# Performance work log

Measured on AMD Instinct MI355X. Metric: run time of the kernel, lower is better.

## Reference

```python
import jax, jax.numpy as jnp
import numpy as np

MODEL_DIMS = 2048
BATCH, SEQ = 4, 4096
NFREQ = MODEL_DIMS // 2 + 1  # rfft spectrum length


def setup_inputs() -> dict:
    key = jax.random.key(0)
    k1, k2, k3, k4 = jax.random.split(key, 4)
    x = jax.random.normal(k1, (BATCH, SEQ, MODEL_DIMS), dtype=jnp.float32)
    queries = jax.random.normal(k2, (1, 1, NFREQ), dtype=jnp.float32)
    keyvalues = jax.random.normal(k3, (1, 1, NFREQ), dtype=jnp.float32)
    # torch nn.Linear(model_dims, model_dims, bias=False): weight is [out, in]
    w_out = jax.random.normal(k4, (MODEL_DIMS, MODEL_DIMS), dtype=jnp.float32) * (MODEL_DIMS ** -0.5)
    return {"x": x, "queries": queries, "keyvalues": keyvalues, "w_out": w_out}


def reference(x, queries, keyvalues, w_out):
    # hrr.fft = rfft over feature dim -> complex64 [B, S, NFREQ]
    xhat = jnp.fft.rfft(x, axis=-1)
    q = xhat * queries            # real spectral params broadcast-multiply
    kv = xhat * keyvalues
    kv = jnp.cumsum(kv, axis=1)   # causal prefix sum over sequence
    qv = q * kv
    values_hat = jnp.fft.irfft(qv, n=x.shape[-1], axis=-1)  # back to real [B, S, D]
    # torch Linear: y = x @ W^T
    return jnp.einsum('bsd,ed->bse', values_hat, w_out)
```

## Files before the change

### kernel.cpp

```cpp
#include <hip/hip_runtime.h>
#include <hip/hip_bf16.h>
#include <stdint.h>

#define BATCH 4
#define SEQ   4096
#define DIM   2048
#define NFREQ 1025
#define NCPLX 1024
#define ROWS  (BATCH*SEQ)

#define SCH  16
#define NSC  (SEQ/SCH)
#define NSCG 16
#define NGRP (NSC/NSCG)

#define SPEC_STRIDE 257

typedef __bf16 bf16x8 __attribute__((ext_vector_type(8)));
typedef float  f32x4  __attribute__((ext_vector_type(4)));

__device__ __forceinline__ int drev4(int n) {
  return ((n&3)<<8) | (((n>>2)&3)<<6) | (((n>>4)&3)<<4) | (((n>>6)&3)<<2) | ((n>>8)&3);
}
#define ZI(i) ((i) + ((i)>>4))

__device__ __forceinline__ float2 cmulf(float2 a, float2 b) {
  return make_float2(a.x*b.x - a.y*b.y, a.x*b.y + a.y*b.x);
}

__device__ __forceinline__ unsigned short f2bf(float f) {
  union { float f; unsigned u; } v; v.f = f;
  unsigned r = v.u + 0x7fffu + ((v.u >> 16) & 1u);
  return (unsigned short)(r >> 16);
}
__device__ __forceinline__ unsigned packbf(float2 v) {
  return (unsigned)f2bf(v.x) | ((unsigned)f2bf(v.y) << 16);
}
__device__ __forceinline__ float2 unpackbf(unsigned u) {
  union { unsigned u; float f; } a, b;
  a.u = u << 16; b.u = u & 0xffff0000u;
  return make_float2(a.f, b.f);
}

template<int INV>
__device__ __forceinline__ void fft_stages_tw(float2* z, int tid, const float2* tw1) {
  {
    int b4 = tid*4;
    float2 x0=z[ZI(b4)], x1=z[ZI(b4+1)], x2=z[ZI(b4+2)], x3=z[ZI(b4+3)];
    float2 a = make_float2(x0.x+x2.x, x0.y+x2.y), b = make_float2(x0.x-x2.x, x0.y-x2.y);
    float2 c = make_float2(x1.x+x3.x, x1.y+x3.y), d = make_float2(x1.x-x3.x, x1.y-x3.y);
    z[ZI(b4)]   = make_float2(a.x+c.x, a.y+c.y);
    z[ZI(b4+2)] = make_float2(a.x-c.x, a.y-c.y);
    if (!INV) { z[ZI(b4+1)] = make_float2(b.x+d.y, b.y-d.x);
                z[ZI(b4+3)] = make_float2(b.x-d.y, b.y+d.x); }
    else      { z[ZI(b4+1)] = make_float2(b.x-d.y, b.y+d.x);
                z[ZI(b4+3)] = make_float2(b.x+d.y, b.y-d.x); }
  }
  __syncthreads();
#pragma unroll
  for (int s = 0; s < 4; ++s) {
    const int lq = 2 + 2*s;
    const int q  = 1 << lq;
    int j = tid & (q-1), g = tid >> lq;
    int base = (g << (lq+2)) + j;
    float2 w1 = tw1[s]; if (INV) w1.y = -w1.y;
    float2 w2 = cmulf(w1, w1), w3 = cmulf(w2, w1);
    float2 x0 = z[ZI(base)];
    float2 x1 = cmulf(z[ZI(base+q)],   w1);
    float2 x2 = cmulf(z[ZI(base+2*q)], w2);
    float2 x3 = cmulf(z[ZI(base+3*q)], w3);
    float2 a = make_float2(x0.x+x2.x, x0.y+x2.y), b = make_float2(x0.x-x2.x, x0.y-x2.y);
    float2 c = make_float2(x1.x+x3.x, x1.y+x3.y), d = make_float2(x1.x-x3.x, x1.y-x3.y);
    z[ZI(base)]     = make_float2(a.x+c.x, a.y+c.y);
    z[ZI(base+2*q)] = make_float2(a.x-c.x, a.y-c.y);
    if (!INV) { z[ZI(base+q)]   = make_float2(b.x+d.y, b.y-d.x);
                z[ZI(base+3*q)] = make_float2(b.x-d.y, b.y+d.x); }
    else      { z[ZI(base+q)]   = make_float2(b.x-d.y, b.y+d.x);
                z[ZI(base+3*q)] = make_float2(b.x+d.y, b.y-d.x); }
    __syncthreads();
  }
}

__device__ __forceinline__ void make_tw1(int tid, float2* tw1) {
#pragma unroll
  for (int s = 0; s < 4; ++s) {
    const int lq = 2 + 2*s;
    const int q  = 1 << lq;
    int j = tid & (q-1);
    float ang = -6.2831853071795864769f * (float)j / (float)(4*q);
    float sw, cw; __sincosf(ang, &sw, &cw);
    tw1[s] = make_float2(cw, sw);
  }
}

__global__ __launch_bounds__(256) void fwd_fused(const float* __restrict__ x,
                                                 const float* __restrict__ kvs,
                                                 uint4* __restrict__ spec,
                                                 float2* __restrict__ partial) {
  __shared__ float2 z[ZI(1023)+2];
  const int tid = threadIdx.x;
  const int sc = blockIdx.x & (NSC-1), b = blockIdx.x >> 8;

  float2 tw1[4];
  make_tw1(tid, tw1);
  const int kA = tid, kB = tid + 256;
  float swA, cwA, swB, cwB;
  __sincosf(-3.14159265358979323846f * (float)kA / 1024.0f, &swA, &cwA);
  __sincosf(-3.14159265358979323846f * (float)kB / 1024.0f, &swB, &cwB);
  int id0 = ZI(drev4(2*tid)),     id1 = ZI(drev4(2*tid+1));
  int id2 = ZI(drev4(2*tid+512)), id3 = ZI(drev4(2*tid+513));

  float2 sA={0,0}, sAp={0,0}, sB={0,0}, sBp={0,0}, s5={0,0};

  const size_t row0 = (size_t)b*SEQ + (size_t)sc*SCH;
  const float* xrow = x + row0*DIM;
  float4 c0 = ((const float4*)xrow)[tid];
  float4 c1 = ((const float4*)xrow)[tid + 256];

  for (int s = 0; s < SCH; ++s) {
    float4 n0f, n1f;
    if (s+1 < SCH) {
      const float* nx = xrow + (size_t)(s+1)*DIM;
      n0f = ((const float4*)nx)[tid]; n1f = ((const float4*)nx)[tid + 256];
    }
    z[id0] = make_float2(c0.x, c0.y); z[id1] = make_float2(c0.z, c0.w);
    z[id2] = make_float2(c1.x, c1.y); z[id3] = make_float2(c1.z, c1.w);
    __syncthreads();
    fft_stages_tw<0>(z, tid, tw1);
    float2 ZkA = z[ZI(kA)], ZnA = z[ZI((NCPLX - kA) & (NCPLX-1))];
    float2 ZkB = z[ZI(kB)], ZnB = z[ZI(768 - tid)];
    float Er = 0.5f*(ZkA.x + ZnA.x), Ei = 0.5f*(ZkA.y - ZnA.y);
    float dr = 0.5f*(ZkA.x - ZnA.x), di = 0.5f*(ZkA.y + ZnA.y);
    float2 vA  = make_float2( Er + cwA*di + swA*dr,  Ei + swA*di - cwA*dr);
    float2 vAp = make_float2( Er - cwA*di - swA*dr, -Ei + swA*di - cwA*dr);
    float Fr = 0.5f*(ZkB.x + ZnB.x), Fi = 0.5f*(ZkB.y - ZnB.y);
    float er = 0.5f*(ZkB.x - ZnB.x), ei = 0.5f*(ZkB.y + ZnB.y);
    float2 vB  = make_float2( Fr + cwB*ei + swB*er,  Fi + swB*ei - cwB*er);
    float2 vBp = make_float2( Fr - cwB*ei - swB*er, -Fi + swB*ei - cwB*er);
    sA.x += vA.x;  sA.y += vA.y;   sAp.x += vAp.x; sAp.y += vAp.y;
    sB.x += vB.x;  sB.y += vB.y;   sBp.x += vBp.x; sBp.y += vBp.y;
    uint4* sprow = spec + (row0 + s) * SPEC_STRIDE;
    sprow[tid] = make_uint4(packbf(vA), packbf(vAp), packbf(vB), packbf(vBp));
    if (tid == 0) {
      float2 Z5 = z[ZI(512)];
      float2 v5 = make_float2(Z5.x, -Z5.y);
      s5.x += v5.x; s5.y += v5.y;
      ((unsigned*)(sprow + 256))[0] = packbf(v5);
    }
    __syncthreads();
    c0 = n0f; c1 = n1f;
  }
  float2* pp = partial + ((size_t)(b*NSC + sc)) * NFREQ;
  float kvA = kvs[kA], kvAp = kvs[NCPLX - kA], kvB = kvs[kB], kvBp = kvs[768 - tid];
  pp[kA]          = make_float2(kvA*sA.x,  kvA*sA.y);
  pp[NCPLX - kA]  = make_float2(kvAp*sAp.x, kvAp*sAp.y);
  pp[kB]          = make_float2(kvB*sB.x,  kvB*sB.y);
  pp[768 - tid]   = make_float2(kvBp*sBp.x, kvBp*sBp.y);
  if (tid == 0) { float kv5 = kvs[512]; pp[512] = make_float2(kv5*s5.x, kv5*s5.y); }
}

__global__ __launch_bounds__(256) void scanA(float2* __restrict__ partial,
                                             float2* __restrict__ gtot) {
  int kc = blockIdx.x % 5, g = (blockIdx.x / 5) % NGRP, b = blockIdx.x / (5*NGRP);
  int k = kc*256 + threadIdx.x;
  if (k >= NFREQ) return;
  float2* p = partial + ((size_t)(b*NSC + g*NSCG)) * NFREQ + k;
  float2 run = {0.f, 0.f};
#pragma unroll
  for (int i = 0; i < NSCG; ++i) {
    float2 t = p[(size_t)i*NFREQ];
    p[(size_t)i*NFREQ] = run;
    run.x += t.x; run.y += t.y;
  }
  gtot[((size_t)(b*NGRP + g)) * NFREQ + k] = run;
}

__global__ __launch_bounds__(256) void scanB(float2* __restrict__ gtot) {
  int kc = blockIdx.x % 5, b = blockIdx.x / 5;
  int k = kc*256 + threadIdx.x;
  if (k >= NFREQ) return;
  float2* p = gtot + ((size_t)b*NGRP) * NFREQ + k;
  float2 run = {0.f, 0.f};
#pragma unroll
  for (int g = 0; g < NGRP; ++g) {
    float2 t = p[(size_t)g*NFREQ];
    p[(size_t)g*NFREQ] = run;
    run.x += t.x; run.y += t.y;
  }
}

__global__ __launch_bounds__(256) void inv_fused(const uint4* __restrict__ spec,
                                                 const float* __restrict__ kvs,
                                                 const float* __restrict__ qs_,
                                                 const float2* __restrict__ partial,
                                                 const float2* __restrict__ gtot,
                                                 unsigned short* __restrict__ vout) {
  __shared__ float2 z[ZI(1023)+2];
  const int tid = threadIdx.x;
  const int sc = blockIdx.x & (NSC-1), b = blockIdx.x >> 8;

  float2 tw1[4];
  make_tw1(tid, tw1);
  const int kA = tid, kB = tid + 256;
  float swA, cwA, swB, cwB;
  __sincosf(3.14159265358979323846f * (float)kA / 1024.0f, &swA, &cwA);
  __sincosf(3.14159265358979323846f * (float)kB / 1024.0f, &swB, &cwB);
  int ridA  = ZI(drev4(kA));
  int ridAp = ZI(drev4((NCPLX - kA) & (NCPLX-1)));
  int ridB  = ZI(drev4(kB));
  int ridBp = ZI(drev4(768 - tid));

  float ksA = kvs[kA], ksAp = kvs[NCPLX - kA], ksB = kvs[kB], ksBp = kvs[768 - tid];
  float qsA = qs_[kA], qsAp = qs_[NCPLX - kA], qsB = qs_[kB], qsBp = qs_[768 - tid];

  const float2* pp = partial + ((size_t)(b*NSC + sc)) * NFREQ;
  const float2* gp = gtot + ((size_t)(b*NGRP + (sc >> 4))) * NFREQ;
  float2 CA  = make_float2(pp[kA].x + gp[kA].x,                 pp[kA].y + gp[kA].y);
  float2 CAp = make_float2(pp[NCPLX-kA].x + gp[NCPLX-kA].x,     pp[NCPLX-kA].y + gp[NCPLX-kA].y);
  float2 CB  = make_float2(pp[kB].x + gp[kB].x,                 pp[kB].y + gp[kB].y);
  float2 CBp = make_float2(pp[768-tid].x + gp[768-tid].x,       pp[768-tid].y + gp[768-tid].y);
  float ks5 = kvs[512], qs5 = qs_[512];
  float2 C5 = make_float2(pp[512].x + gp[512].x, pp[512].y + gp[512].y);
  const int rid5 = ZI(drev4(512));

  const size_t row0 = (size_t)b*SEQ + (size_t)sc*SCH;
  const uint4* sprow = spec + row0 * SPEC_STRIDE;
  unsigned* vr = (unsigned*)(vout + row0 * DIM);
  uint4 sp = sprow[tid];
  unsigned spN = ((const unsigned*)(sprow + 256))[0];
  const float scl = 1.0f/1024.0f;

  for (int s = 0; s < SCH; ++s) {
    uint4 spn; unsigned spNn;
    if (s+1 < SCH) {
      const uint4* nr = sprow + (size_t)(s+1) * SPEC_STRIDE;
      spn = nr[tid]; spNn = ((const unsigned*)(nr + 256))[0];
    }
    float2 vA = unpackbf(sp.x), vAp = unpackbf(sp.y);
    float2 vB = unpackbf(sp.z), vBp = unpackbf(sp.w);
    CA.x  += vA.x*ksA;   CA.y  += vA.y*ksA;
    CAp.x += vAp.x*ksAp; CAp.y += vAp.y*ksAp;
    CB.x  += vB.x*ksB;   CB.y  += vB.y*ksB;
    CBp.x += vBp.x*ksBp; CBp.y += vBp.y*ksBp;
    float2 qvA  = make_float2(qsA *(vA.x*CA.x  - vA.y*CA.y),  qsA *(vA.x*CA.y  + vA.y*CA.x));
    float2 qvAp = make_float2(qsAp*(vAp.x*CAp.x- vAp.y*CAp.y),qsAp*(vAp.x*CAp.y+ vAp.y*CAp.x));
    float2 qvB  = make_float2(qsB *(vB.x*CB.x  - vB.y*CB.y),  qsB *(vB.x*CB.y  + vB.y*CB.x));
    float2 qvBp = make_float2(qsBp*(vBp.x*CBp.x- vBp.y*CBp.y),qsBp*(vBp.x*CBp.y+ vBp.y*CBp.x));
    float Er = 0.5f*(qvA.x + qvAp.x), Ei = 0.5f*(qvA.y - qvAp.y);
    float dr = 0.5f*(qvA.x - qvAp.x), di = 0.5f*(qvA.y + qvAp.y);
    float Or = dr*cwA - di*swA, Oi = dr*swA + di*cwA;
    float2 valA  = make_float2(scl*(Er - Oi), scl*( Ei + Or));
    float2 valAp = make_float2(scl*(Er + Oi), scl*(-Ei + Or));
    float Fr = 0.5f*(qvB.x + qvBp.x), Fi = 0.5f*(qvB.y - qvBp.y);
    float er = 0.5f*(qvB.x - qvBp.x), ei = 0.5f*(qvB.y + qvBp.y);
    float Pr = er*cwB - ei*swB, Pi = er*swB + ei*cwB;
    float2 valB  = make_float2(scl*(Fr - Pi), scl*( Fi + Pr));
    float2 valBp = make_float2(scl*(Fr + Pi), scl*(-Fi + Pr));
    z[ridA] = valA; z[ridAp] = valAp; z[ridB] = valB; z[ridBp] = valBp;
    if (tid == 0) {
      float2 v5 = unpackbf(spN);
      C5.x += v5.x*ks5; C5.y += v5.y*ks5;
      float2 qv5 = make_float2(qs5*(v5.x*C5.x - v5.y*C5.y), qs5*(v5.x*C5.y + v5.y*C5.x));
      z[rid5] = make_float2(scl*qv5.x, -scl*qv5.y);
    }
    __syncthreads();
    fft_stages_tw<1>(z, tid, tw1);
    unsigned* vr32 = vr + (size_t)s * (DIM/2);
#pragma unroll
    for (int i = 0; i < 4; ++i) {
      int n = tid + 256*i;
      float2 t2 = z[ZI(n)];
      vr32[n] = packbf(t2);
    }
    __syncthreads();
    sp = spn; spN = spNn;
  }
}

__global__ __launch_bounds__(256) void w_to_bf16(const float* __restrict__ w,
                                                 unsigned short* __restrict__ wb) {
  size_t idx = (size_t)blockIdx.x * 256 + threadIdx.x;
  float4 v = ((const float4*)w)[idx];
  uint2 o;
  o.x = (unsigned)f2bf(v.x) | ((unsigned)f2bf(v.y) << 16);
  o.y = (unsigned)f2bf(v.z) | ((unsigned)f2bf(v.w) << 16);
  ((uint2*)wb)[idx] = o;
}

#define NKT (DIM/64)
#define NIT (NKT/2)

#define BARX() do{ __builtin_amdgcn_s_barrier(); __builtin_amdgcn_sched_barrier(0); }while(0)
#define VMW(N) do{ asm volatile("s_waitcnt vmcnt(" #N ")" ::: "memory"); __builtin_amdgcn_sched_barrier(0); }while(0)

#define LOADA(B_, MH) do{ _Pragma("unroll") for (int m_=0;m_<4;++m_) _Pragma("unroll") for (int kk_=0;kk_<2;++kk_){ \
    int rA_ = wm*64 + m_*16 + l15; \
    aF[m_][kk_] = *(const bf16x8*)(smem + ((B_)*2+(MH))*16384 + rA_*128 + ((kk_*64 + lhi*16) ^ ((rA_&7)<<4))); } }while(0)

#define LOADB(DST, B_, NH) do{ _Pragma("unroll") for (int n_=0;n_<2;++n_) _Pragma("unroll") for (int kk_=0;kk_<2;++kk_){ \
    int rB_ = wn*32 + n_*16 + l15; \
    DST[n_][kk_] = *(const bf16x8*)(smem + 65536 + ((B_)*2+(NH))*16384 + rB_*128 + ((kk_*64 + lhi*16) ^ ((rB_&7)<<4))); } }while(0)

#define MM(MH, NH, BF) do{ __builtin_amdgcn_s_setprio(1); \
    _Pragma("unroll") for (int kk_=0;kk_<2;++kk_) _Pragma("unroll") for (int m_=0;m_<4;++m_) _Pragma("unroll") for (int n_=0;n_<2;++n_) \
      acc[MH][NH][m_][n_] = __builtin_amdgcn_mfma_f32_16x16x32_bf16(aF[m_][kk_], BF[n_][kk_], acc[MH][NH][m_][n_], 0, 0, 0); \
    __builtin_amdgcn_s_setprio(0); }while(0)

#define STAGEH(REG, B_, H_, GP, ROW0, KT) do{ _Pragma("unroll") for (int c_=0;c_<2;++c_){ \
    int ci_ = c_*512 + tid; int r_ = ci_>>3, sl_ = ci_&7; \
    const unsigned short* sp_ = (GP) + (size_t)((ROW0) + (H_)*128 + r_)*DIM + (KT) + ((sl_ ^ (r_&7))*8); \
    __builtin_amdgcn_global_load_lds((const __attribute__((address_space(1))) void*)sp_, \
      (__attribute__((address_space(3))) void*)(smem + (REG) + ((B_)*2+(H_))*16384 + ci_*16), 16, 0, 0); } }while(0)

__global__ __launch_bounds__(512, 2) void gemm256(const unsigned short* __restrict__ A,
                                                  const unsigned short* __restrict__ B,
                                                  float* __restrict__ C) {
  __shared__ __align__(16) char smem[131072];
  const int tid = threadIdx.x;
  const int lane = tid & 63;
  const int wid  = tid >> 6;
  const int wm = wid >> 2, wn = wid & 3;
  const int l15 = lane & 15, lhi = lane >> 4;

  const int bn = blockIdx.x & 7, bm = blockIdx.x >> 3;
  const int m0 = bm * 256, n0 = bn * 256;

  f32x4 acc[2][2][4][2] = {};
  bf16x8 aF[4][2], bF0[2][2], bF1[2][2];

  STAGEH(0,     0,0, A, m0, 0);  STAGEH(65536, 0,0, B, n0, 0);
  STAGEH(65536, 0,1, B, n0, 0);  STAGEH(0,     0,1, A, m0, 0);
  STAGEH(0,     1,0, A, m0, 64); STAGEH(65536, 1,0, B, n0, 64);
  STAGEH(65536, 1,1, B, n0, 64); STAGEH(0,     1,1, A, m0, 64);
  VMW(8);
  BARX();

#pragma unroll 1
  for (int j = 0; j < NIT-1; ++j) {
    const int kA = (2*j+2)*64, kB = (2*j+3)*64;
    LOADA(0,0); LOADB(bF0, 0,0);
    BARX(); MM(0,0,bF0); BARX();
    LOADB(bF1, 0,1);
    STAGEH(0, 0,0, A, m0, kA); STAGEH(65536, 0,0, B, n0, kA);
    BARX(); MM(0,1,bF1); BARX();
    LOADA(0,1);
    STAGEH(65536, 0,1, B, n0, kA);
    BARX(); MM(1,0,bF0); BARX();
    STAGEH(0, 0,1, A, m0, kA);
    VMW(8);
    BARX(); MM(1,1,bF1); BARX();
    LOADA(1,0); LOADB(bF0, 1,0);
    BARX(); MM(0,0,bF0); BARX();
    LOADB(bF1, 1,1);
    STAGEH(0, 1,0, A, m0, kB); STAGEH(65536, 1,0, B, n0, kB);
    BARX(); MM(0,1,bF1); BARX();
    LOADA(1,1);
    STAGEH(65536, 1,1, B, n0, kB);
    BARX(); MM(1,0,bF0); BARX();
    STAGEH(0, 1,1, A, m0, kB);
    VMW(8);
    BARX(); MM(1,1,bF1); BARX();
  }
  LOADA(0,0); LOADB(bF0, 0,0);
  BARX(); MM(0,0,bF0); BARX();
  LOADB(bF1, 0,1);
  BARX(); MM(0,1,bF1); BARX();
  LOADA(0,1);
  BARX(); MM(1,0,bF0); BARX();
  VMW(0);
  BARX(); MM(1,1,bF1); BARX();
  LOADA(1,0); LOADB(bF0, 1,0);
  BARX(); MM(0,0,bF0); BARX();
  LOADB(bF1, 1,1);
  BARX(); MM(0,1,bF1); BARX();
  LOADA(1,1);
  BARX(); MM(1,0,bF0); BARX();
  BARX(); MM(1,1,bF1); BARX();

  const int crow = lhi * 4;
#pragma unroll
  for (int mh = 0; mh < 2; ++mh)
#pragma unroll
    for (int nh = 0; nh < 2; ++nh)
#pragma unroll
      for (int m_ = 0; m_ < 4; ++m_)
#pragma unroll
        for (int n_ = 0; n_ < 2; ++n_) {
          float* cp = C + (size_t)(m0 + mh*128 + wm*64 + m_*16 + crow) * DIM
                        + (n0 + nh*128 + wn*32 + n_*16 + l15);
#pragma unroll
          for (int j2 = 0; j2 < 4; ++j2)
            cp[(size_t)j2 * DIM] = acc[mh][nh][m_][n_][j2];
        }
}

extern "C" void kernel_launch(void* const* d_in, const int* in_sizes, int n_in,
                              void* d_out, int out_size, void* d_ws, size_t ws_size,
                              hipStream_t stream) {
  const float* x    = (const float*)d_in[0];
  const float* qry  = (const float*)d_in[1];
  const float* kvs  = (const float*)d_in[2];
  const float* wout = (const float*)d_in[3];
  float* out = (float*)d_out;

  char* ws = (char*)d_ws;
  size_t off = 0;
  uint4* spec = (uint4*)(ws + off);
  off += (size_t)ROWS * SPEC_STRIDE * sizeof(uint4);
  off = (off + 255) & ~(size_t)255;
  unsigned short* vbf = (unsigned short*)(ws + off);
  off += (size_t)ROWS * DIM * sizeof(unsigned short);
  off = (off + 255) & ~(size_t)255;
  unsigned short* wbf = (unsigned short*)(ws + off);
  off += (size_t)DIM * DIM * sizeof(unsigned short);
  off = (off + 255) & ~(size_t)255;
  float2* partial = (float2*)(ws + off);
  off += (size_t)BATCH * NSC * NFREQ * sizeof(float2);
  off = (off + 255) & ~(size_t)255;
  float2* gtot = (float2*)(ws + off);
  off += (size_t)BATCH * NGRP * NFREQ * sizeof(float2);

  hipLaunchKernelGGL(w_to_bf16, dim3((DIM*DIM)/(256*4)), dim3(256), 0, stream, wout, wbf);
  hipLaunchKernelGGL(fwd_fused, dim3(BATCH*NSC),         dim3(256), 0, stream, x, kvs, spec, partial);
  hipLaunchKernelGGL(scanA,     dim3(BATCH*NGRP*5),      dim3(256), 0, stream, partial, gtot);
  hipLaunchKernelGGL(scanB,     dim3(BATCH*5),           dim3(256), 0, stream, gtot);
  hipLaunchKernelGGL(inv_fused, dim3(BATCH*NSC),         dim3(256), 0, stream, spec, kvs, qry, partial, gtot, vbf);
  hipLaunchKernelGGL(gemm256,   dim3((ROWS/256)*(DIM/256)), dim3(512), 0, stream, vbf, wbf, out);
}
```

Measured before the change: 248.6 us.

## Fold the inverse real FFT into the output projection weights

Instead of running an inverse FFT on every activation row, the change applies a forward real FFT to each row of the weight matrix, scaled so the spectrum rows act as the irfft basis. The inverse kernel now only writes the spectral product's real and imaginary parts as bf16 straight into the GEMM input, which removes the per-row FFT stages, twiddle setup and extra shared-memory passes. The cost is a per-call FFT over the 2048 weight rows, plus extra rounding because spectral values go through bf16 before the matmul. The GEMM block-to-tile mapping is also remapped, probably for cache locality.

```diff
diff --git a/kernel.cpp b/kernel.cpp
--- a/kernel.cpp
+++ b/kernel.cpp
@@ -159,6 +159,63 @@
   if (tid == 0) { float kv5 = kvs[512]; pp[512] = make_float2(kv5*s5.x, kv5*s5.y); }
 }
 
+__global__ __launch_bounds__(256) void wfft(const float* __restrict__ w,
+                                            unsigned short* __restrict__ H) {
+  __shared__ float2 z[ZI(1023)+2];
+  __shared__ __align__(16) unsigned short hrow[2048];
+  const int tid = threadIdx.x;
+  const int e = blockIdx.x;
+
+  float2 tw1[4];
+  make_tw1(tid, tw1);
+  const int kB = tid + 256;
+  float swA, cwA, swB, cwB;
+  __sincosf(-3.14159265358979323846f * (float)tid / 1024.0f, &swA, &cwA);
+  __sincosf(-3.14159265358979323846f * (float)kB  / 1024.0f, &swB, &cwB);
+  int id0 = ZI(drev4(2*tid)),     id1 = ZI(drev4(2*tid+1));
+  int id2 = ZI(drev4(2*tid+512)), id3 = ZI(drev4(2*tid+513));
+
+  const float* wr = w + (size_t)e * DIM;
+  float4 c0 = ((const float4*)wr)[tid];
+  float4 c1 = ((const float4*)wr)[tid + 256];
+  z[id0] = make_float2(c0.x, c0.y); z[id1] = make_float2(c0.z, c0.w);
+  z[id2] = make_float2(c1.x, c1.y); z[id3] = make_float2(c1.z, c1.w);
+  __syncthreads();
+  fft_stages_tw<0>(z, tid, tw1);
+
+  float2 ZkA = z[ZI(tid)], ZnA = z[ZI((NCPLX - tid) & (NCPLX-1))];
+  float2 ZkB = z[ZI(kB)],  ZnB = z[ZI(768 - tid)];
+  float Er = 0.5f*(ZkA.x + ZnA.x), Ei = 0.5f*(ZkA.y - ZnA.y);
+  float dr = 0.5f*(ZkA.x - ZnA.x), di = 0.5f*(ZkA.y + ZnA.y);
+  float2 vA  = make_float2( Er + cwA*di + swA*dr,  Ei + swA*di - cwA*dr);
+  float2 vAp = make_float2( Er - cwA*di - swA*dr, -Ei + swA*di - cwA*dr);
+  float Fr = 0.5f*(ZkB.x + ZnB.x), Fi = 0.5f*(ZkB.y - ZnB.y);
+  float er = 0.5f*(ZkB.x - ZnB.x), ei = 0.5f*(ZkB.y + ZnB.y);
+  float2 vB  = make_float2( Fr + cwB*ei + swB*er,  Fi + swB*ei - cwB*er);
+  float2 vBp = make_float2( Fr - cwB*ei - swB*er, -Fi + swB*ei - cwB*er);
+
+  const float invN = 1.0f/2048.0f, twoN = 2.0f/2048.0f;
+  float aA  = (tid == 0) ? invN : twoN;
+  float aAp = (tid == 0) ? invN : twoN;
+  hrow[tid]        = f2bf(aA  * vA.x);
+  hrow[1024 - tid] = f2bf(aAp * vAp.x);
+  hrow[256 + tid]  = f2bf(twoN * vB.x);
+  hrow[768 - tid]  = f2bf(twoN * vBp.x);
+  if (tid) {
+    hrow[1024 + tid] = f2bf(twoN * vA.y);
+    hrow[2048 - tid] = f2bf(twoN * vAp.y);
+  }
+  hrow[1280 + tid] = f2bf(twoN * vB.y);
+  hrow[1792 - tid] = f2bf(twoN * vBp.y);
+  if (tid == 0) {
+    float2 Z5 = z[ZI(512)];
+    hrow[512]  = f2bf(twoN * Z5.x);
+    hrow[1536] = f2bf(twoN * (-Z5.y));
+  }
+  __syncthreads();
+  ((uint4*)(H + (size_t)e * DIM))[tid] = ((const uint4*)hrow)[tid];
+}
+
 __global__ __launch_bounds__(256) void scanA(float2* __restrict__ partial,
                                              float2* __restrict__ gtot) {
   int kc = blockIdx.x % 5, g = (blockIdx.x / 5) % NGRP, b = blockIdx.x / (5*NGRP);
@@ -194,21 +251,11 @@
                                                  const float* __restrict__ qs_,
                                                  const float2* __restrict__ partial,
                                                  const float2* __restrict__ gtot,
-                                                 unsigned short* __restrict__ vout) {
-  __shared__ float2 z[ZI(1023)+2];
+                                                 unsigned short* __restrict__ G) {
+  __shared__ __align__(16) unsigned short grow[2048];
   const int tid = threadIdx.x;
   const int sc = blockIdx.x & (NSC-1), b = blockIdx.x >> 8;
-
-  float2 tw1[4];
-  make_tw1(tid, tw1);
   const int kA = tid, kB = tid + 256;
-  float swA, cwA, swB, cwB;
-  __sincosf(3.14159265358979323846f * (float)kA / 1024.0f, &swA, &cwA);
-  __sincosf(3.14159265358979323846f * (float)kB / 1024.0f, &swB, &cwB);
-  int ridA  = ZI(drev4(kA));
-  int ridAp = ZI(drev4((NCPLX - kA) & (NCPLX-1)));
-  int ridB  = ZI(drev4(kB));
-  int ridBp = ZI(drev4(768 - tid));
 
   float ksA = kvs[kA], ksAp = kvs[NCPLX - kA], ksB = kvs[kB], ksBp = kvs[768 - tid];
   float qsA = qs_[kA], qsAp = qs_[NCPLX - kA], qsB = qs_[kB], qsBp = qs_[768 - tid];
@@ -221,14 +268,11 @@
   float2 CBp = make_float2(pp[768-tid].x + gp[768-tid].x,       pp[768-tid].y + gp[768-tid].y);
   float ks5 = kvs[512], qs5 = qs_[512];
   float2 C5 = make_float2(pp[512].x + gp[512].x, pp[512].y + gp[512].y);
-  const int rid5 = ZI(drev4(512));
 
   const size_t row0 = (size_t)b*SEQ + (size_t)sc*SCH;
   const uint4* sprow = spec + row0 * SPEC_STRIDE;
-  unsigned* vr = (unsigned*)(vout + row0 * DIM);
   uint4 sp = sprow[tid];
   unsigned spN = ((const unsigned*)(sprow + 256))[0];
-  const float scl = 1.0f/1024.0f;
 
   for (int s = 0; s < SCH; ++s) {
     uint4 spn; unsigned spNn;
@@ -246,45 +290,27 @@
     float2 qvAp = make_float2(qsAp*(vAp.x*CAp.x- vAp.y*CAp.y),qsAp*(vAp.x*CAp.y+ vAp.y*CAp.x));
     float2 qvB  = make_float2(qsB *(vB.x*CB.x  - vB.y*CB.y),  qsB *(vB.x*CB.y  + vB.y*CB.x));
     float2 qvBp = make_float2(qsBp*(vBp.x*CBp.x- vBp.y*CBp.y),qsBp*(vBp.x*CBp.y+ vBp.y*CBp.x));
-    float Er = 0.5f*(qvA.x + qvAp.x), Ei = 0.5f*(qvA.y - qvAp.y);
-    float dr = 0.5f*(qvA.x - qvAp.x), di = 0.5f*(qvA.y + qvAp.y);
-    float Or = dr*cwA - di*swA, Oi = dr*swA + di*cwA;
-    float2 valA  = make_float2(scl*(Er - Oi), scl*( Ei + Or));
-    float2 valAp = make_float2(scl*(Er + Oi), scl*(-Ei + Or));
-    float Fr = 0.5f*(qvB.x + qvBp.x), Fi = 0.5f*(qvB.y - qvBp.y);
-    float er = 0.5f*(qvB.x - qvBp.x), ei = 0.5f*(qvB.y + qvBp.y);
-    float Pr = er*cwB - ei*swB, Pi = er*swB + ei*cwB;
-    float2 valB  = make_float2(scl*(Fr - Pi), scl*( Fi + Pr));
-    float2 valBp = make_float2(scl*(Fr + Pi), scl*(-Fi + Pr));
-    z[ridA] = valA; z[ridAp] = valAp; z[ridB] = valB; z[ridBp] = valBp;
+    grow[tid]        = f2bf(qvA.x);
+    grow[1024 - tid] = f2bf(qvAp.x);
+    grow[256 + tid]  = f2bf(qvB.x);
+    grow[768 - tid]  = f2bf(qvBp.x);
+    if (tid) {
+      grow[1024 + tid] = f2bf(qvA.y);
+      grow[2048 - tid] = f2bf(qvAp.y);
+    }
+    grow[1280 + tid] = f2bf(qvB.y);
+    grow[1792 - tid] = f2bf(qvBp.y);
     if (tid == 0) {
       float2 v5 = unpackbf(spN);
       C5.x += v5.x*ks5; C5.y += v5.y*ks5;
-      float2 qv5 = make_float2(qs5*(v5.x*C5.x - v5.y*C5.y), qs5*(v5.x*C5.y + v5.y*C5.x));
-      z[rid5] = make_float2(scl*qv5.x, -scl*qv5.y);
+      grow[512]  = f2bf(qs5*(v5.x*C5.x - v5.y*C5.y));
+      grow[1536] = f2bf(qs5*(v5.x*C5.y + v5.y*C5.x));
     }
     __syncthreads();
-    fft_stages_tw<1>(z, tid, tw1);
-    unsigned* vr32 = vr + (size_t)s * (DIM/2);
-#pragma unroll
-    for (int i = 0; i < 4; ++i) {
-      int n = tid + 256*i;
-      float2 t2 = z[ZI(n)];
-      vr32[n] = packbf(t2);
-    }
+    ((uint4*)(G + (row0 + s) * DIM))[tid] = ((const uint4*)grow)[tid];
     __syncthreads();
     sp = spn; spN = spNn;
   }
-}
-
-__global__ __launch_bounds__(256) void w_to_bf16(const float* __restrict__ w,
-                                                 unsigned short* __restrict__ wb) {
-  size_t idx = (size_t)blockIdx.x * 256 + threadIdx.x;
-  float4 v = ((const float4*)w)[idx];
-  uint2 o;
-  o.x = (unsigned)f2bf(v.x) | ((unsigned)f2bf(v.y) << 16);
-  o.y = (unsigned)f2bf(v.z) | ((unsigned)f2bf(v.w) << 16);
-  ((uint2*)wb)[idx] = o;
 }
 
 #define NKT (DIM/64)
@@ -322,7 +348,8 @@
   const int wm = wid >> 2, wn = wid & 3;
   const int l15 = lane & 15, lhi = lane >> 4;
 
-  const int bn = blockIdx.x & 7, bm = blockIdx.x >> 3;
+  const int xj = blockIdx.x & 7, tt = blockIdx.x >> 3;
+  const int bm = xj * 8 + (tt >> 3), bn = tt & 7;
   const int m0 = bm * 256, n0 = bn * 256;
 
   f32x4 acc[2][2][4][2] = {};
@@ -408,10 +435,10 @@
   uint4* spec = (uint4*)(ws + off);
   off += (size_t)ROWS * SPEC_STRIDE * sizeof(uint4);
   off = (off + 255) & ~(size_t)255;
-  unsigned short* vbf = (unsigned short*)(ws + off);
+  unsigned short* G = (unsigned short*)(ws + off);
   off += (size_t)ROWS * DIM * sizeof(unsigned short);
   off = (off + 255) & ~(size_t)255;
-  unsigned short* wbf = (unsigned short*)(ws + off);
+  unsigned short* H = (unsigned short*)(ws + off);
   off += (size_t)DIM * DIM * sizeof(unsigned short);
   off = (off + 255) & ~(size_t)255;
   float2* partial = (float2*)(ws + off);
@@ -420,10 +447,10 @@
   float2* gtot = (float2*)(ws + off);
   off += (size_t)BATCH * NGRP * NFREQ * sizeof(float2);
 
-  hipLaunchKernelGGL(w_to_bf16, dim3((DIM*DIM)/(256*4)), dim3(256), 0, stream, wout, wbf);
+  hipLaunchKernelGGL(wfft,      dim3(DIM),               dim3(256), 0, stream, wout, H);
   hipLaunchKernelGGL(fwd_fused, dim3(BATCH*NSC),         dim3(256), 0, stream, x, kvs, spec, partial);
   hipLaunchKernelGGL(scanA,     dim3(BATCH*NGRP*5),      dim3(256), 0, stream, partial, gtot);
   hipLaunchKernelGGL(scanB,     dim3(BATCH*5),           dim3(256), 0, stream, gtot);
-  hipLaunchKernelGGL(inv_fused, dim3(BATCH*NSC),         dim3(256), 0, stream, spec, kvs, qry, partial, gtot, vbf);
-  hipLaunchKernelGGL(gemm256,   dim3((ROWS/256)*(DIM/256)), dim3(512), 0, stream, vbf, wbf, out);
-}
+  hipLaunchKernelGGL(inv_fused, dim3(BATCH*NSC),         dim3(256), 0, stream, spec, kvs, qry, partial, gtot, G);
+  hipLaunchKernelGGL(gemm256,   dim3((ROWS/256)*(DIM/256)), dim3(512), 0, stream, G, H, out);
+}
```

After: 222.9 us. 1.12x faster.
